# Performance work log

Hardware: AMD Instinct MI355X
Metric: run time of the kernel (lower is better)

## Reference

```python
import jax, jax.numpy as jnp
import numpy as np

B, CH, H, W, D = 2, 32, 256, 512, 192


def setup_inputs() -> dict:
    key = jax.random.key(0)
    ks = jax.random.split(key, 10)
    def w(k, shape, fan_in):
        return jax.random.normal(k, shape, jnp.float32) * (1.0 / np.sqrt(fan_in))
    return {
        "x": jax.random.normal(ks[0], (B, CH, H, W), jnp.float32),
        "y": jax.random.normal(ks[1], (B, CH, H, W), jnp.float32),
        # encoder: 1x1 convs ch->64->32->1 (shared for x and y)
        "w1": w(ks[2], (64, CH), CH), "b1": w(ks[3], (64,), CH),
        "w2": w(ks[4], (32, 64), 64), "b2": w(ks[5], (32,), 64),
        "w3": w(ks[6], (1, 32), 32), "b3": w(ks[7], (1,), 32),
        # decoderl: 1x1 conv maxdisp->maxdisp (original code applies decoderl to BOTH volumes)
        "wd": w(ks[8], (D, D), D), "bd": w(ks[9], (D,), D),
    }


def _conv1x1(w, b, h):  # [O,C] x [B,C,H,W] -> [B,O,H,W]
    return jnp.einsum("oc,bchw->bohw", w, h) + b[None, :, None, None]


def _encoder(x, w1, b1, w2, b2, w3, b3):
    h = jax.nn.relu(x)
    h = jax.nn.relu(_conv1x1(w1, b1, h))
    h = jax.nn.relu(_conv1x1(w2, b2, h))
    h = jax.nn.relu(_conv1x1(w3, b3, h))
    return h[:, 0]  # squeeze channel -> [B,H,W]


def _cost_volumes(xf, yf):
    # costx[b,d,h,w] = xf[b,h,w+d] * yf[b,h,w]   (0 where w+d >= W)
    # costy[b,d,h,w] = xf[b,h,w]   * yf[b,h,w-d] (0 where w-d < 0)
    dgrid = jnp.arange(D)
    wgrid = jnp.arange(W)
    x_pad = jnp.pad(xf, ((0, 0), (0, 0), (0, D)))          # zero pad right
    xg = x_pad[:, :, wgrid[None, :] + dgrid[:, None]]       # [B,H,D,W]
    costx = (xg * yf[:, :, None, :]).transpose(0, 2, 1, 3)  # [B,D,H,W]
    y_pad = jnp.pad(yf, ((0, 0), (0, 0), (D, 0)))           # zero pad left
    yg = y_pad[:, :, wgrid[None, :] - dgrid[:, None] + D]   # [B,H,D,W]
    costy = (xf[:, :, None, :] * yg).transpose(0, 2, 1, 3)  # [B,D,H,W]
    return costx, costy


def reference(x, y, w1, b1, w2, b2, w3, b3, wd, bd):
    xf = _encoder(x, w1, b1, w2, b2, w3, b3)
    yf = _encoder(y, w1, b1, w2, b2, w3, b3)
    costx, costy = _cost_volumes(xf, yf)
    probx = jax.nn.softmax(_conv1x1(wd, bd, costx), axis=1)
    proby = jax.nn.softmax(_conv1x1(wd, bd, costy), axis=1)  # decoderl used for both, as in source
    disp_vals = jnp.arange(D, dtype=probx.dtype)
    dispx = jnp.einsum("bdhw,d->bhw", probx, disp_vals)
    dispy = jnp.einsum("bdhw,d->bhw", proby, disp_vals)
    return dispx, dispy
```

## Files before the change

kernel.cpp:

```cpp
#include <hip/hip_runtime.h>


typedef __attribute__((ext_vector_type(8)))  __bf16 bf16x8;
typedef __attribute__((ext_vector_type(4)))  float  f32x4;
typedef __attribute__((ext_vector_type(16))) float  f32x16;

#define MFMA32(a,b,c) __builtin_amdgcn_mfma_f32_32x32x16_bf16((a),(b),(c),0,0,0)
#define MFMA16(a,b,c) __builtin_amdgcn_mfma_f32_16x16x32_bf16((a),(b),(c),0,0,0)

constexpr int WW  = 512;
constexpr int HW  = 256 * 512;
constexpr int CHW = 32 * HW;
constexpr float LOG2E = 1.4426950408889634f;

constexpr size_t XFB_OFF = 0;
constexpr int    STB     = 25600;
constexpr size_t WDP_OFF = 2 * 262144 * 2;
constexpr size_t BDP_OFF = WDP_OFF + 3 * STB;

__global__ __launch_bounds__(512)
void panet_encode(const float* __restrict__ gx,  const float* __restrict__ gy,
                  const float* __restrict__ gw1, const float* __restrict__ gb1,
                  const float* __restrict__ gw2, const float* __restrict__ gb2,
                  const float* __restrict__ gw3, const float* __restrict__ gb3,
                  const float* __restrict__ gwd, const float* __restrict__ gbd,
                  char* __restrict__ ws)
{
  const int blk = blockIdx.x;
  const int tid = threadIdx.x;

  if (blk >= 1024) {
    const int pi = blk - 1024;
    unsigned short* wdp = (unsigned short*)(ws + WDP_OFF);
    for (int idx = tid; idx < 12 * 200; idx += 512) {
      const int oo = idx / 200;
      const int k  = idx - oo * 200;
      const int o  = 12 * pi + oo;
      const int stage = o >> 6;
      const int r     = o & 63;
      unsigned short v = 0;
      if (k < 192) v = __builtin_bit_cast(unsigned short, (__bf16)gwd[o * 192 + k]);
      wdp[stage * 12800 + r * 200 + k] = v;
    }
    if (pi == 0) {
      float* bdp = (float*)(ws + BDP_OFF);
      if (tid < 192) bdp[tid] = gbd[tid] * LOG2E;
    }
    return;
  }

  const int t    = blk >> 9;
  const int bh   = blk & 511;
  const int lane = tid & 63;
  const int m    = lane & 15;
  const int g    = lane >> 4;
  const int wid  = tid >> 6;

  bf16x8 A1[4], A2[2][2];
  f32x4  bias1[4], bias2[2], w3v[2];
  #pragma unroll
  for (int Mt = 0; Mt < 4; ++Mt) {
    const float* p = gw1 + (16 * Mt + m) * 32 + 4 * g;
    const f32x4 u0 = *(const f32x4*)p;
    const f32x4 u1 = *(const f32x4*)(p + 16);
    #pragma unroll
    for (int j = 0; j < 4; ++j) { A1[Mt][j] = (__bf16)u0[j]; A1[Mt][j + 4] = (__bf16)u1[j]; }
    bias1[Mt] = *(const f32x4*)(gb1 + 16 * Mt + 4 * g);
  }
  #pragma unroll
  for (int Mt = 0; Mt < 2; ++Mt) {
    #pragma unroll
    for (int s = 0; s < 2; ++s) {
      const float* p = gw2 + (16 * Mt + m) * 64 + 32 * s + 4 * g;
      const f32x4 u0 = *(const f32x4*)p;
      const f32x4 u1 = *(const f32x4*)(p + 16);
      #pragma unroll
      for (int j = 0; j < 4; ++j) { A2[Mt][s][j] = (__bf16)u0[j]; A2[Mt][s][j + 4] = (__bf16)u1[j]; }
    }
    bias2[Mt] = *(const f32x4*)(gb2 + 16 * Mt + 4 * g);
    w3v[Mt]   = *(const f32x4*)(gw3 + 16 * Mt + 4 * g);
  }
  const float b3s = gb3[0];
  const f32x4 zf4 = {0.f, 0.f, 0.f, 0.f};
  const float* base = (t ? gy : gx) + (bh >> 8) * CHW + (bh & 255) * WW;
  unsigned short* xfb = (unsigned short*)(ws + XFB_OFF) + t * 262144 + bh * 512;

  for (int u = wid; u < 32; u += 8) {
    const int w0 = u << 4;
    const float* src = base + w0 + m;

    bf16x8 B1;
    #pragma unroll
    for (int j = 0; j < 8; ++j) {
      const int c = 16 * (j >> 2) + 4 * g + (j & 3);
      B1[j] = (__bf16)fmaxf(src[c * HW], 0.f);
    }
    f32x4 acc1[4];
    #pragma unroll
    for (int Mt = 0; Mt < 4; ++Mt) acc1[Mt] = MFMA16(A1[Mt], B1, zf4);

    bf16x8 B2[2];
    #pragma unroll
    for (int s = 0; s < 2; ++s) {
      #pragma unroll
      for (int j = 0; j < 4; ++j) {
        B2[s][j]     = (__bf16)fmaxf(acc1[2 * s][j]     + bias1[2 * s][j],     0.f);
        B2[s][j + 4] = (__bf16)fmaxf(acc1[2 * s + 1][j] + bias1[2 * s + 1][j], 0.f);
      }
    }
    f32x4 acc2[2];
    #pragma unroll
    for (int Mt = 0; Mt < 2; ++Mt)
      acc2[Mt] = MFMA16(A2[Mt][1], B2[1], MFMA16(A2[Mt][0], B2[0], zf4));

    float s3 = 0.f;
    #pragma unroll
    for (int Mt = 0; Mt < 2; ++Mt)
      #pragma unroll
      for (int r = 0; r < 4; ++r)
        s3 += w3v[Mt][r] * fmaxf(acc2[Mt][r] + bias2[Mt][r], 0.f);
    s3 += __shfl_xor(s3, 16);
    s3 += __shfl_xor(s3, 32);
    const float val = fmaxf(s3 + b3s, 0.f);

    if (lane < 16)
      xfb[w0 + m] = __builtin_bit_cast(unsigned short, (__bf16)val);
  }
}

constexpr int CPS    = 1424;
constexpr int K2_WD  = 0;
constexpr int K2_HK  = 2 * STB;
constexpr int K2_BD  = K2_HK + 11392;
constexpr int K2_LDS = K2_BD + 768;

__global__ __launch_bounds__(512)
void panet_corr(const char* __restrict__ ws, float* __restrict__ gout)
{
  __shared__ __align__(16) char lds[K2_LDS];
  const int blk  = blockIdx.x;
  const int dir  = blk >> 9;
  const int bh   = blk & 511;
  const int tid  = threadIdx.x;
  const int lane = tid & 63;
  const int l31  = lane & 31;
  const int h    = lane >> 5;
  const int wid  = tid >> 6;

  const unsigned short* xfb = (const unsigned short*)(ws + XFB_OFF);
  const unsigned short* hs = xfb + (dir ? 262144 : 0) + bh * 512;
  const unsigned short* ss = xfb + (dir ? 0 : 262144) + bh * 512;

  f32x4 streg[4];

  {
    const char* src = ws + WDP_OFF;
    #pragma unroll
    for (int k = 0; k < 3; ++k) streg[k] = *(const f32x4*)(src + (tid + 512 * k) * 16);
    if (tid < 64) streg[3] = *(const f32x4*)(src + (tid + 1536) * 16);

    int* zp = (int*)(lds + K2_HK);
    for (int i = tid; i < 11392 / 4; i += 512) zp[i] = 0;
    const float* bdp = (const float*)(ws + BDP_OFF);
    if (tid < 192) ((float*)(lds + K2_BD))[tid] = bdp[tid];
  }
  __syncthreads();
  #pragma unroll
  for (int c = 0; c < 8; ++c) {
    const int e = tid;
    if (e + c <= 511)
      ((unsigned short*)(lds + K2_HK + c * CPS))[e] = hs[dir ? (511 - e - c) : (e + c)];
  }
  {
    char* dst = lds + K2_WD;
    #pragma unroll
    for (int k = 0; k < 3; ++k) *(f32x4*)(dst + (tid + 512 * k) * 16) = streg[k];
    if (tid < 64) *(f32x4*)(dst + (tid + 1536) * 16) = streg[3];
  }
  __syncthreads();

  int bfb[2]; float sc[2];
  #pragma unroll
  for (int ct = 0; ct < 2; ++ct) {
    const int col = wid * 64 + ct * 32 + l31;
    const int I0  = dir ? (511 - col) : col;
    const int cc  = I0 & 7;
    bfb[ct] = K2_HK + cc * CPS + 2 * (I0 - cc) + 16 * h;
    sc[ct]  = LOG2E * __builtin_bit_cast(float, (unsigned)ss[col] << 16);
  }
  const int baseA = l31 * 400 + 16 * h;

  float stM[2] = {-3.4e38f, -3.4e38f};
  float stS[2] = {0.f, 0.f};
  float stW[2] = {0.f, 0.f};

  for (int s = 0; s < 3; ++s) {
    if (s < 2) {
      const char* src = ws + WDP_OFF + (s + 1) * STB;
      #pragma unroll
      for (int k = 0; k < 3; ++k) streg[k] = *(const f32x4*)(src + (tid + 512 * k) * 16);
      if (tid < 64) streg[3] = *(const f32x4*)(src + (tid + 1536) * 16);
    }

    const int bufo = (s & 1) * STB;
    f32x16 a00 = {0}, a01 = {0}, a10 = {0}, a11 = {0};
    #pragma unroll 2
    for (int ks = 0; ks < 12; ++ks) {
      const int ko = 32 * ks;
      const bf16x8 af0 = *(const bf16x8*)(lds + K2_WD + bufo + baseA + ko);
      const bf16x8 af1 = *(const bf16x8*)(lds + K2_WD + bufo + baseA + 12800 + ko);
      const bf16x8 bf0 = *(const bf16x8*)(lds + bfb[0] + ko);
      const bf16x8 bf1 = *(const bf16x8*)(lds + bfb[1] + ko);
      a00 = MFMA32(af0, bf0, a00);
      a01 = MFMA32(af0, bf1, a01);
      a10 = MFMA32(af1, bf0, a10);
      a11 = MFMA32(af1, bf1, a11);
    }

    #pragma unroll
    for (int ct = 0; ct < 2; ++ct) {
      const f32x16 A0 = ct ? a01 : a00;
      const f32x16 A1 = ct ? a11 : a10;
      float L0[16], L1[16];
      #pragma unroll
      for (int q = 0; q < 4; ++q) {
        const f32x4 bd0 = *(const f32x4*)(lds + K2_BD + (64 * s + 8 * q + 4 * h) * 4);
        const f32x4 bd1 = *(const f32x4*)(lds + K2_BD + (64 * s + 8 * q + 4 * h + 32) * 4);
        #pragma unroll
        for (int r = 0; r < 4; ++r) {
          L0[4 * q + r] = fmaf(sc[ct], A0[4 * q + r], bd0[r]);
          L1[4 * q + r] = fmaf(sc[ct], A1[4 * q + r], bd1[r]);
        }
      }
      float t[16];
      #pragma unroll
      for (int i = 0; i < 16; ++i) t[i] = fmaxf(L0[i], L1[i]);
      #pragma unroll
      for (int off = 8; off > 0; off >>= 1)
        #pragma unroll
        for (int i = 0; i < off; ++i) t[i] = fmaxf(t[i], t[i + off]);
      const float nm   = fmaxf(stM[ct], t[0]);
      const float fold = exp2f(stM[ct] - nm);
      float lsp[4] = {0.f, 0.f, 0.f, 0.f}, lwp[4] = {0.f, 0.f, 0.f, 0.f};
      #pragma unroll
      for (int i = 0; i < 16; ++i) {
        const float c  = (float)((i & 3) + 8 * (i >> 2));
        const float p0 = exp2f(L0[i] - nm);
        const float p1 = exp2f(L1[i] - nm);
        lsp[i & 3] += p0 + p1;
        lwp[i & 3] = fmaf(c, p0, lwp[i & 3]);
        lwp[i & 3] = fmaf(c + 32.f, p1, lwp[i & 3]);
      }
      float ls = (lsp[0] + lsp[1]) + (lsp[2] + lsp[3]);
      float lw = (lwp[0] + lwp[1]) + (lwp[2] + lwp[3]);
      lw = fmaf((float)(64 * s + 4 * h), ls, lw);
      stS[ct] = fmaf(stS[ct], fold, ls);
      stW[ct] = fmaf(stW[ct], fold, lw);
      stM[ct] = nm;
    }

    if (s < 2) {
      char* dst = lds + K2_WD + ((s + 1) & 1) * STB;
      #pragma unroll
      for (int k = 0; k < 3; ++k) *(f32x4*)(dst + (tid + 512 * k) * 16) = streg[k];
      if (tid < 64) *(f32x4*)(dst + (tid + 1536) * 16) = streg[3];
      __syncthreads();
    }
  }

  float* outp = gout + dir * 262144 + bh * 512;
  #pragma unroll
  for (int ct = 0; ct < 2; ++ct) {
    const float Mo = __shfl_xor(stM[ct], 32);
    const float M  = fmaxf(stM[ct], Mo);
    const float f  = exp2f(stM[ct] - M);
    float sr = stS[ct] * f;
    float wr = stW[ct] * f;
    sr += __shfl_xor(sr, 32);
    wr += __shfl_xor(wr, 32);
    if (lane < 32) outp[wid * 64 + ct * 32 + l31] = wr / sr;
  }
}

extern "C" void kernel_launch(void* const* d_in, const int* in_sizes, int n_in,
                              void* d_out, int out_size, void* d_ws, size_t ws_size,
                              hipStream_t stream) {
  const float* x  = (const float*)d_in[0];
  const float* y  = (const float*)d_in[1];
  const float* w1 = (const float*)d_in[2];
  const float* b1 = (const float*)d_in[3];
  const float* w2 = (const float*)d_in[4];
  const float* b2 = (const float*)d_in[5];
  const float* w3 = (const float*)d_in[6];
  const float* b3 = (const float*)d_in[7];
  const float* wd = (const float*)d_in[8];
  const float* bd = (const float*)d_in[9];
  char* ws = (char*)d_ws;

  panet_encode<<<1040, 512, 0, stream>>>(x, y, w1, b1, w2, b2, w3, b3, wd, bd, ws);
  panet_corr<<<1024, 512, 0, stream>>>(ws, (float*)d_out);
}
```

Before: 83.70 us.

## Split corr rows across two 256-thread blocks with single-buffered weight stage

The correlation kernel now launches 2048 blocks of 256 threads, each covering half a row's columns. The weight stage in LDS is single-buffered, with two barriers per stage, which frees about 25KB of shared memory per block so more blocks can be resident on a CU. The exp2f calls become the raw hardware exp2 builtin to drop range-handling code. In exchange, each row's weights and shifted-input staging are now loaded twice, the extra barriers add synchronisation cost, and the register staging array grows.

```diff
diff --git a/kernel.cpp b/kernel.cpp
--- a/kernel.cpp
+++ b/kernel.cpp
@@ -130,17 +130,18 @@
 
 constexpr int CPS    = 1424;
 constexpr int K2_WD  = 0;
-constexpr int K2_HK  = 2 * STB;
+constexpr int K2_HK  = STB;
 constexpr int K2_BD  = K2_HK + 11392;
 constexpr int K2_LDS = K2_BD + 768;
 
-__global__ __launch_bounds__(512)
+__global__ __launch_bounds__(256)
 void panet_corr(const char* __restrict__ ws, float* __restrict__ gout)
 {
   __shared__ __align__(16) char lds[K2_LDS];
   const int blk  = blockIdx.x;
-  const int dir  = blk >> 9;
-  const int bh   = blk & 511;
+  const int dir  = blk >> 10;
+  const int bh   = (blk >> 1) & 511;
+  const int ch2  = blk & 1;
   const int tid  = threadIdx.x;
   const int lane = tid & 63;
   const int l31  = lane & 31;
@@ -151,38 +152,45 @@
   const unsigned short* hs = xfb + (dir ? 262144 : 0) + bh * 512;
   const unsigned short* ss = xfb + (dir ? 0 : 262144) + bh * 512;
 
-  f32x4 streg[4];
+  f32x4 streg[7];
 
   {
     const char* src = ws + WDP_OFF;
     #pragma unroll
-    for (int k = 0; k < 3; ++k) streg[k] = *(const f32x4*)(src + (tid + 512 * k) * 16);
-    if (tid < 64) streg[3] = *(const f32x4*)(src + (tid + 1536) * 16);
+    for (int k = 0; k < 6; ++k) streg[k] = *(const f32x4*)(src + (tid + 256 * k) * 16);
+    if (tid < 64) streg[6] = *(const f32x4*)(src + (tid + 1536) * 16);
 
     int* zp = (int*)(lds + K2_HK);
-    for (int i = tid; i < 11392 / 4; i += 512) zp[i] = 0;
+    for (int i = tid; i < 11392 / 4; i += 256) zp[i] = 0;
     const float* bdp = (const float*)(ws + BDP_OFF);
     if (tid < 192) ((float*)(lds + K2_BD))[tid] = bdp[tid];
   }
   __syncthreads();
   #pragma unroll
-  for (int c = 0; c < 8; ++c) {
-    const int e = tid;
-    if (e + c <= 511)
-      ((unsigned short*)(lds + K2_HK + c * CPS))[e] = hs[dir ? (511 - e - c) : (e + c)];
+  for (int e0 = 0; e0 < 512; e0 += 256) {
+    const int e = e0 + tid;
+    #pragma unroll
+    for (int c = 0; c < 8; ++c) {
+      if (e + c <= 511)
+        ((unsigned short*)(lds + K2_HK + c * CPS))[e] = hs[dir ? (511 - e - c) : (e + c)];
+    }
   }
   {
     char* dst = lds + K2_WD;
     #pragma unroll
-    for (int k = 0; k < 3; ++k) *(f32x4*)(dst + (tid + 512 * k) * 16) = streg[k];
-    if (tid < 64) *(f32x4*)(dst + (tid + 1536) * 16) = streg[3];
+    for (int k = 0; k < 6; ++k) *(f32x4*)(dst + (tid + 256 * k) * 16) = streg[k];
+    if (tid < 64) *(f32x4*)(dst + (tid + 1536) * 16) = streg[6];
+    const char* src = ws + WDP_OFF + STB;
+    #pragma unroll
+    for (int k = 0; k < 6; ++k) streg[k] = *(const f32x4*)(src + (tid + 256 * k) * 16);
+    if (tid < 64) streg[6] = *(const f32x4*)(src + (tid + 1536) * 16);
   }
   __syncthreads();
 
   int bfb[2]; float sc[2];
   #pragma unroll
   for (int ct = 0; ct < 2; ++ct) {
-    const int col = wid * 64 + ct * 32 + l31;
+    const int col = ch2 * 256 + wid * 64 + ct * 32 + l31;
     const int I0  = dir ? (511 - col) : col;
     const int cc  = I0 & 7;
     bfb[ct] = K2_HK + cc * CPS + 2 * (I0 - cc) + 16 * h;
@@ -195,20 +203,12 @@
   float stW[2] = {0.f, 0.f};
 
   for (int s = 0; s < 3; ++s) {
-    if (s < 2) {
-      const char* src = ws + WDP_OFF + (s + 1) * STB;
-      #pragma unroll
-      for (int k = 0; k < 3; ++k) streg[k] = *(const f32x4*)(src + (tid + 512 * k) * 16);
-      if (tid < 64) streg[3] = *(const f32x4*)(src + (tid + 1536) * 16);
-    }
-
-    const int bufo = (s & 1) * STB;
     f32x16 a00 = {0}, a01 = {0}, a10 = {0}, a11 = {0};
     #pragma unroll 2
     for (int ks = 0; ks < 12; ++ks) {
       const int ko = 32 * ks;
-      const bf16x8 af0 = *(const bf16x8*)(lds + K2_WD + bufo + baseA + ko);
-      const bf16x8 af1 = *(const bf16x8*)(lds + K2_WD + bufo + baseA + 12800 + ko);
+      const bf16x8 af0 = *(const bf16x8*)(lds + K2_WD + baseA + ko);
+      const bf16x8 af1 = *(const bf16x8*)(lds + K2_WD + baseA + 12800 + ko);
       const bf16x8 bf0 = *(const bf16x8*)(lds + bfb[0] + ko);
       const bf16x8 bf1 = *(const bf16x8*)(lds + bfb[1] + ko);
       a00 = MFMA32(af0, bf0, a00);
@@ -240,13 +240,13 @@
         #pragma unroll
         for (int i = 0; i < off; ++i) t[i] = fmaxf(t[i], t[i + off]);
       const float nm   = fmaxf(stM[ct], t[0]);
-      const float fold = exp2f(stM[ct] - nm);
+      const float fold = __builtin_amdgcn_exp2f(stM[ct] - nm);
       float lsp[4] = {0.f, 0.f, 0.f, 0.f}, lwp[4] = {0.f, 0.f, 0.f, 0.f};
       #pragma unroll
       for (int i = 0; i < 16; ++i) {
         const float c  = (float)((i & 3) + 8 * (i >> 2));
-        const float p0 = exp2f(L0[i] - nm);
-        const float p1 = exp2f(L1[i] - nm);
+        const float p0 = __builtin_amdgcn_exp2f(L0[i] - nm);
+        const float p1 = __builtin_amdgcn_exp2f(L1[i] - nm);
         lsp[i & 3] += p0 + p1;
         lwp[i & 3] = fmaf(c, p0, lwp[i & 3]);
         lwp[i & 3] = fmaf(c + 32.f, p1, lwp[i & 3]);
@@ -260,20 +260,27 @@
     }
 
     if (s < 2) {
-      char* dst = lds + K2_WD + ((s + 1) & 1) * STB;
-      #pragma unroll
-      for (int k = 0; k < 3; ++k) *(f32x4*)(dst + (tid + 512 * k) * 16) = streg[k];
-      if (tid < 64) *(f32x4*)(dst + (tid + 1536) * 16) = streg[3];
       __syncthreads();
-    }
-  }
-
-  float* outp = gout + dir * 262144 + bh * 512;
+      char* dst = lds + K2_WD;
+      #pragma unroll
+      for (int k = 0; k < 6; ++k) *(f32x4*)(dst + (tid + 256 * k) * 16) = streg[k];
+      if (tid < 64) *(f32x4*)(dst + (tid + 1536) * 16) = streg[6];
+      if (s == 0) {
+        const char* src = ws + WDP_OFF + 2 * STB;
+        #pragma unroll
+        for (int k = 0; k < 6; ++k) streg[k] = *(const f32x4*)(src + (tid + 256 * k) * 16);
+        if (tid < 64) streg[6] = *(const f32x4*)(src + (tid + 1536) * 16);
+      }
+      __syncthreads();
+    }
+  }
+
+  float* outp = gout + dir * 262144 + bh * 512 + ch2 * 256;
   #pragma unroll
   for (int ct = 0; ct < 2; ++ct) {
     const float Mo = __shfl_xor(stM[ct], 32);
     const float M  = fmaxf(stM[ct], Mo);
-    const float f  = exp2f(stM[ct] - M);
+    const float f  = __builtin_amdgcn_exp2f(stM[ct] - M);
     float sr = stS[ct] * f;
     float wr = stW[ct] * f;
     sr += __shfl_xor(sr, 32);
@@ -298,5 +305,5 @@
   char* ws = (char*)d_ws;
 
   panet_encode<<<1040, 512, 0, stream>>>(x, y, w1, b1, w2, b2, w3, b3, wd, bd, ws);
-  panet_corr<<<1024, 512, 0, stream>>>(ws, (float*)d_out);
+  panet_corr<<<2048, 256, 0, stream>>>(ws, (float*)d_out);
 }
```

New measurement: 80.33 us. 1.04x faster.
